# Kernel tuning notes

Measured on AMD Instinct MI355X. Metric: run time of the kernel, lower is better.

The kernel has to match this reference:

```python
import jax, jax.numpy as jnp
import numpy as np
import math

B = 8192       # batch (tokens)
HID = 4096     # hidden size
H = 32         # num query heads
KV = 8         # num kv heads
GQA = H // KV  # 4
D = 128        # head dim
RBIT = 128     # hash bits
QKV = (H + 2 * KV) * D  # 6144


def setup_inputs() -> dict:
    key = jax.random.key(0)
    k1, k2, k3 = jax.random.split(key, 3)
    hidden = jax.random.normal(k1, (B, HID), jnp.float32)
    proj_w = jax.random.normal(k2, (HID, QKV), jnp.float32) * 0.02
    proj_b = jnp.zeros((QKV,), jnp.float32)
    # xavier_uniform init for hash weight [D, RBIT]
    limit = math.sqrt(6.0 / (D + RBIT))
    hash_w = jax.random.uniform(k3, (D, RBIT), jnp.float32, -limit, limit)
    return {"hidden": hidden, "proj_w": proj_w, "proj_b": proj_b, "hash_w": hash_w}


def reference(hidden, proj_w, proj_b, hash_w):
    # fused qkv projection
    qkv = hidden @ proj_w + proj_b                     # [B, QKV]
    q = qkv[:, : H * D].reshape(B, H, D)               # [B, H, D]
    k = qkv[:, H * D : (H + KV) * D].reshape(B, KV, 1, D)
    k = jnp.broadcast_to(k, (B, KV, GQA, D)).reshape(B, H, D)  # GQA expand

    inv_sqrt_d = 1.0 / math.sqrt(D)
    attn_weights = jnp.einsum("bhd,bhd->bh", q, k) * inv_sqrt_d  # with_norm=True

    # hash codes: BinaryStochastic (training mode): (tanh(x)+1)/2
    q_code = (jnp.tanh(q @ hash_w) + 1.0) * 0.5        # [B, H, RBIT]
    k_code = (jnp.tanh(k @ hash_w) + 1.0) * 0.5
    ham_dist = jnp.abs(q_code - k_code).sum(axis=-1)   # [B, H]
    ham_weights = 1.0 - 2.0 * ham_dist / RBIT

    # with_norm: scale by |q| |k| / sqrt(D)
    q_norm = jnp.linalg.norm(q, axis=-1)
    k_norm = jnp.linalg.norm(k, axis=-1)
    ham_weights = ham_weights * q_norm * k_norm * inv_sqrt_d

    return attn_weights.reshape(-1), ham_weights.reshape(-1)
```

## Files before the change

### kernel.cpp

```cpp
#include <hip/hip_runtime.h>
#include <hip/hip_bf16.h>
#include <cstdint>
#include <cstddef>

#define B_TOK 8192
#define HID   4096
#define NH    32
#define NKV   8
#define DH    128
#define RB    128
#define KDIM  4096
#define NOUT  5120
#define QKVW  6144

typedef __bf16 bf16x8 __attribute__((ext_vector_type(8)));
typedef __bf16 bf16x4 __attribute__((ext_vector_type(4)));
typedef float  f32x4  __attribute__((ext_vector_type(4)));

__device__ __forceinline__ void async_ld16(const void* g, void* l) {
  __builtin_amdgcn_global_load_lds(
      (__attribute__((address_space(1))) void*)(g),
      (__attribute__((address_space(3))) void*)(l), 16, 0, 0);
}

__device__ __forceinline__ float code_of(float x) {
  const float e = exp2f(x * -2.885390081777927f);
  return __builtin_amdgcn_rcpf(1.0f + e);
}


#define NB_HID  16384
#define NB_WT   5120
#define NB_HASH 64

__global__ void prep_kernel(const float* __restrict__ hidden, __bf16* __restrict__ Abf,
                            const float* __restrict__ W, __bf16* __restrict__ Wt,
                            const float* __restrict__ hw, __bf16* __restrict__ hwT) {
  __shared__ float t[64][65];
  const int bx  = blockIdx.x;
  const int tid = threadIdx.x;

  if (bx < NB_HID) {
    const int i = bx * 256 + tid;
    const float4 v0 = ((const float4*)hidden)[2 * i];
    const float4 v1 = ((const float4*)hidden)[2 * i + 1];
    bf16x8 o;
    o[0] = (__bf16)v0.x; o[1] = (__bf16)v0.y; o[2] = (__bf16)v0.z; o[3] = (__bf16)v0.w;
    o[4] = (__bf16)v1.x; o[5] = (__bf16)v1.y; o[6] = (__bf16)v1.z; o[7] = (__bf16)v1.w;
    ((bf16x8*)Abf)[i] = o;
  } else if (bx < NB_HID + NB_WT) {
    const int bt = bx - NB_HID;
    const int n0 = (bt % 80) * 64;
    const int k0 = (bt / 80) * 64;
    const int c  = tid & 63;
    const int r0 = tid >> 6;
#pragma unroll
    for (int j = 0; j < 16; ++j) {
      const int r = r0 + j * 4;
      t[r][c] = W[(size_t)(k0 + r) * QKVW + n0 + c];
    }
    __syncthreads();
#pragma unroll
    for (int j = 0; j < 16; ++j) {
      const int n = r0 + j * 4;
      Wt[(size_t)(n0 + n) * KDIM + k0 + c] = (__bf16)t[c][n];
    }
  } else {
    const int idx = (bx - NB_HID - NB_WT) * 256 + tid;
    const int r = idx >> 7;
    const int d = idx & 127;
    hwT[r * RB + d] = (__bf16)hw[(size_t)d * RB + r];
  }
}


__global__ void gemm_qk(const __bf16* __restrict__ A,
                        const __bf16* __restrict__ Bt,
                        const float* __restrict__ bias,
                        __bf16* __restrict__ C) {
  __shared__ __bf16 As[128 * 32];
  __shared__ __bf16 Bs[128 * 32];

  const int tid  = threadIdx.x;
  const int lane = tid & 63;
  const int wave = tid >> 6;
  const int m0 = blockIdx.y * 128;
  const int n0 = blockIdx.x * 128;
  const int waveM = (wave >> 1) * 64;
  const int waveN = (wave & 1) * 64;

  const int srow  = lane >> 2;
  const int selem = (lane & 3) * 8;

  const __bf16* ga0 = A + (size_t)(m0 + wave * 16 + srow) * KDIM + selem;
  const __bf16* ga1 = ga0 + (size_t)64 * KDIM;
  const __bf16* gb0 = Bt + (size_t)(n0 + wave * 16 + srow) * KDIM + selem;
  const __bf16* gb1 = gb0 + (size_t)64 * KDIM;
  __bf16* la0 = As + wave * 512;
  __bf16* la1 = As + (wave + 4) * 512;
  __bf16* lb0 = Bs + wave * 512;
  __bf16* lb1 = Bs + (wave + 4) * 512;

  const int fr = lane & 15;
  const int fk = (lane >> 4) * 8;

  f32x4 acc[4][4] = {};

  for (int kt = 0; kt < KDIM / 32; ++kt) {
    const int k0 = kt * 32;
    async_ld16(ga0 + k0, la0);
    async_ld16(ga1 + k0, la1);
    async_ld16(gb0 + k0, lb0);
    async_ld16(gb1 + k0, lb1);
    __syncthreads();

    bf16x8 af[4], bfr[4];
#pragma unroll
    for (int mi = 0; mi < 4; ++mi)
      af[mi] = *(const bf16x8*)(As + (waveM + mi * 16 + fr) * 32 + fk);
#pragma unroll
    for (int ni = 0; ni < 4; ++ni)
      bfr[ni] = *(const bf16x8*)(Bs + (waveN + ni * 16 + fr) * 32 + fk);
#pragma unroll
    for (int mi = 0; mi < 4; ++mi)
#pragma unroll
      for (int ni = 0; ni < 4; ++ni)
        acc[mi][ni] = __builtin_amdgcn_mfma_f32_16x16x32_bf16(af[mi], bfr[ni],
                                                              acc[mi][ni], 0, 0, 0);
    __syncthreads();
  }

  const int cl = lane & 15;
  const int rq = (lane >> 4) * 4;
#pragma unroll
  for (int ni = 0; ni < 4; ++ni) {
    const int gn = n0 + waveN + ni * 16 + cl;
    const float bb = bias[gn];
#pragma unroll
    for (int mi = 0; mi < 4; ++mi) {
      const int gm = m0 + waveM + mi * 16 + rq;
#pragma unroll
      for (int r = 0; r < 4; ++r)
        C[(size_t)(gm + r) * NOUT + gn] = (__bf16)(acc[mi][ni][r] + bb);
    }
  }
}


__global__ void phase2_kernel(const __bf16* __restrict__ QK,
                              const __bf16* __restrict__ hwT,
                              float* __restrict__ out) {
  __shared__ __bf16 As[48][136];
  __shared__ float code[40][132];
  __shared__ float rednorm[40];
  __shared__ float reddot[32];

  const int tid  = threadIdx.x;
  const int lane = tid & 63;
  const int wave = tid >> 6;
  const int b = blockIdx.x;

  const __bf16* src = QK + (size_t)b * NOUT;
  for (int i = tid; i < 640; i += 256) {
    const int row = i >> 4;
    const int col = (i & 15) * 8;
    *(uint4*)(&As[row][col]) = *(const uint4*)(src + i * 8);
  }

  const int fr = lane & 15;
  const int fk = (lane >> 4) * 8;
  bf16x8 bf[2][4];
#pragma unroll
  for (int nn = 0; nn < 2; ++nn) {
    const int ni = wave + nn * 4;
#pragma unroll
    for (int ks = 0; ks < 4; ++ks)
      bf[nn][ks] = *(const bf16x8*)(hwT + (size_t)(ni * 16 + fr) * RB + ks * 32 + fk);
  }
  __syncthreads();

#pragma unroll
  for (int mi = 0; mi < 3; ++mi) {
    bf16x8 af[4];
#pragma unroll
    for (int ks = 0; ks < 4; ++ks)
      af[ks] = *(const bf16x8*)(&As[mi * 16 + fr][ks * 32 + fk]);
#pragma unroll
    for (int nn = 0; nn < 2; ++nn) {
      const int ni = wave + nn * 4;
      f32x4 acc = {0.f, 0.f, 0.f, 0.f};
#pragma unroll
      for (int ks = 0; ks < 4; ++ks)
        acc = __builtin_amdgcn_mfma_f32_16x16x32_bf16(af[ks], bf[nn][ks], acc, 0, 0, 0);
      const int row0 = mi * 16 + (lane >> 4) * 4;
      const int col  = ni * 16 + (lane & 15);
#pragma unroll
      for (int r = 0; r < 4; ++r) {
        const int row = row0 + r;
        if (row < 40) code[row][col] = code_of(acc[r]);
      }
    }
  }

  {
    const int q = lane >> 4;
    const int c = lane & 15;
    const int ti = (wave == 1 || wave == 3) ? 1 : 0;
    const int tj = (wave >= 2) ? 2 : ti;
    bf16x8 fa[4], fb[4];
#pragma unroll
    for (int ks = 0; ks < 4; ++ks) {
      fa[ks] = *(const bf16x8*)(&As[ti * 16 + fr][ks * 32 + fk]);
      fb[ks] = *(const bf16x8*)(&As[tj * 16 + fr][ks * 32 + fk]);
    }
    f32x4 g = {0.f, 0.f, 0.f, 0.f};
#pragma unroll
    for (int ks = 0; ks < 4; ++ks)
      g = __builtin_amdgcn_mfma_f32_16x16x32_bf16(fa[ks], fb[ks], g, 0, 0, 0);
    if (ti == tj) {
      if ((c >> 2) == q) rednorm[ti * 16 + c] = g[c & 3];
    } else {
      if (c == ti * 4 + q) {
#pragma unroll
        for (int r = 0; r < 4; ++r) reddot[ti * 16 + q * 4 + r] = g[r];
      }
    }
    if (wave == 0) {
      bf16x8 fc[4];
#pragma unroll
      for (int ks = 0; ks < 4; ++ks)
        fc[ks] = *(const bf16x8*)(&As[32 + fr][ks * 32 + fk]);
      f32x4 g2 = {0.f, 0.f, 0.f, 0.f};
#pragma unroll
      for (int ks = 0; ks < 4; ++ks)
        g2 = __builtin_amdgcn_mfma_f32_16x16x32_bf16(fc[ks], fc[ks], g2, 0, 0, 0);
      if ((c >> 2) == q && c < 8) rednorm[32 + c] = g2[c & 3];
    }
  }
  __syncthreads();

  const int h   = tid >> 3;
  const int sub = tid & 7;
  const int kr  = 32 + (h >> 2);
  float s = 0.f;
#pragma unroll
  for (int j = 0; j < 16; ++j) {
    const int c = sub + 8 * j;
    s += fabsf(code[h][c] - code[kr][c]);
  }
  s += __shfl_down(s, 4, 8);
  s += __shfl_down(s, 2, 8);
  s += __shfl_down(s, 1, 8);
  if (sub == 0) {
    const float invsq = 0.08838834764831843f;
    out[(size_t)b * NH + h] = reddot[h] * invsq;
    const float hamw = (1.0f - s * (1.0f / 64.0f)) *
                       sqrtf(rednorm[h]) * sqrtf(rednorm[kr]) * invsq;
    out[(size_t)(B_TOK * NH) + (size_t)b * NH + h] = hamw;
  }
}


extern "C" void kernel_launch(void* const* d_in, const int* in_sizes, int n_in,
                              void* d_out, int out_size, void* d_ws, size_t ws_size,
                              hipStream_t stream) {
  const float* hidden = (const float*)d_in[0];
  const float* proj_w = (const float*)d_in[1];
  const float* proj_b = (const float*)d_in[2];
  const float* hash_w = (const float*)d_in[3];
  float* out = (float*)d_out;

  char* w = (char*)d_ws;
  __bf16* Abf = (__bf16*)(w);
  __bf16* Wt  = (__bf16*)(w + 67108864);
  __bf16* QK  = (__bf16*)(w + 67108864 + 41943040);
  __bf16* hwT = (__bf16*)(w + 67108864 + 41943040 + 83886080);

  prep_kernel<<<NB_HID + NB_WT + NB_HASH, 256, 0, stream>>>(hidden, Abf, proj_w, Wt,
                                                            hash_w, hwT);
  gemm_qk<<<dim3(NOUT / 128, B_TOK / 128), 256, 0, stream>>>(Abf, Wt, proj_b, QK);
  phase2_kernel<<<B_TOK, 256, 0, stream>>>(QK, hwT, out);
}
```

Before: 685.0 us.

## Vectorize weight transpose, double K-step per barrier, remap GEMM tiles per XCD

The weight transpose in the prep kernel now reads float4 rows and writes bf16x8 vectors instead of scalar elements, to cut the number of memory transactions. The GEMM main loop now loads a K=64 slab per iteration into two LDS buffers, halving the number of barrier pairs per tile. The block index is also remapped so that each XCD handles a contiguous group of N tiles, aiming to improve L2 reuse of the weight tiles. The price is twice the LDS per block, which may lower occupancy, and a tile mapping that assumes a 40-wide grid.

New measurement: 630.7 us. 7.9% less time.

```diff
diff --git a/kernel.cpp b/kernel.cpp
--- a/kernel.cpp
+++ b/kernel.cpp
@@ -52,18 +52,25 @@
     const int bt = bx - NB_HID;
     const int n0 = (bt % 80) * 64;
     const int k0 = (bt / 80) * 64;
-    const int c  = tid & 63;
-    const int r0 = tid >> 6;
-#pragma unroll
-    for (int j = 0; j < 16; ++j) {
-      const int r = r0 + j * 4;
-      t[r][c] = W[(size_t)(k0 + r) * QKVW + n0 + c];
+    const int c4 = tid & 15;
+    const int rr = tid >> 4;
+#pragma unroll
+    for (int j = 0; j < 4; ++j) {
+      const int r = rr + j * 16;
+      const float4 v = *(const float4*)&W[(size_t)(k0 + r) * QKVW + n0 + c4 * 4];
+      t[r][c4 * 4 + 0] = v.x; t[r][c4 * 4 + 1] = v.y;
+      t[r][c4 * 4 + 2] = v.z; t[r][c4 * 4 + 3] = v.w;
     }
     __syncthreads();
-#pragma unroll
-    for (int j = 0; j < 16; ++j) {
-      const int n = r0 + j * 4;
-      Wt[(size_t)(n0 + n) * KDIM + k0 + c] = (__bf16)t[c][n];
+    const int c8 = tid & 7;
+    const int nn = tid >> 3;
+#pragma unroll
+    for (int jj = 0; jj < 2; ++jj) {
+      const int n = nn + jj * 32;
+      bf16x8 o;
+#pragma unroll
+      for (int i = 0; i < 8; ++i) o[i] = (__bf16)t[c8 * 8 + i][n];
+      *(bf16x8*)&Wt[(size_t)(n0 + n) * KDIM + k0 + c8 * 8] = o;
     }
   } else {
     const int idx = (bx - NB_HID - NB_WT) * 256 + tid;
@@ -78,14 +85,19 @@
                         const __bf16* __restrict__ Bt,
                         const float* __restrict__ bias,
                         __bf16* __restrict__ C) {
-  __shared__ __bf16 As[128 * 32];
-  __shared__ __bf16 Bs[128 * 32];
+  __shared__ __bf16 As[2][128 * 32];
+  __shared__ __bf16 Bs[2][128 * 32];
 
   const int tid  = threadIdx.x;
   const int lane = tid & 63;
   const int wave = tid >> 6;
-  const int m0 = blockIdx.y * 128;
-  const int n0 = blockIdx.x * 128;
+
+  const int lin = blockIdx.y * 40 + blockIdx.x;
+  const int xcd = lin & 7;
+  const int seq = lin >> 3;
+  const int n0 = (xcd * 5 + (seq % 5)) * 128;
+  const int m0 = (seq / 5) * 128;
+
   const int waveM = (wave >> 1) * 64;
   const int waveN = (wave & 1) * 64;
 
@@ -96,37 +108,44 @@
   const __bf16* ga1 = ga0 + (size_t)64 * KDIM;
   const __bf16* gb0 = Bt + (size_t)(n0 + wave * 16 + srow) * KDIM + selem;
   const __bf16* gb1 = gb0 + (size_t)64 * KDIM;
-  __bf16* la0 = As + wave * 512;
-  __bf16* la1 = As + (wave + 4) * 512;
-  __bf16* lb0 = Bs + wave * 512;
-  __bf16* lb1 = Bs + (wave + 4) * 512;
+  __bf16* la0 = &As[0][wave * 512];
+  __bf16* la1 = &As[0][(wave + 4) * 512];
+  __bf16* lb0 = &Bs[0][wave * 512];
+  __bf16* lb1 = &Bs[0][(wave + 4) * 512];
+  __bf16* la0b = &As[1][wave * 512];
+  __bf16* la1b = &As[1][(wave + 4) * 512];
+  __bf16* lb0b = &Bs[1][wave * 512];
+  __bf16* lb1b = &Bs[1][(wave + 4) * 512];
 
   const int fr = lane & 15;
   const int fk = (lane >> 4) * 8;
 
   f32x4 acc[4][4] = {};
 
-  for (int kt = 0; kt < KDIM / 32; ++kt) {
-    const int k0 = kt * 32;
-    async_ld16(ga0 + k0, la0);
-    async_ld16(ga1 + k0, la1);
-    async_ld16(gb0 + k0, lb0);
-    async_ld16(gb1 + k0, lb1);
+  for (int kt = 0; kt < KDIM / 64; ++kt) {
+    const int k0 = kt * 64;
+    async_ld16(ga0 + k0, la0);  async_ld16(ga0 + k0 + 32, la0b);
+    async_ld16(ga1 + k0, la1);  async_ld16(ga1 + k0 + 32, la1b);
+    async_ld16(gb0 + k0, lb0);  async_ld16(gb0 + k0 + 32, lb0b);
+    async_ld16(gb1 + k0, lb1);  async_ld16(gb1 + k0 + 32, lb1b);
     __syncthreads();
 
-    bf16x8 af[4], bfr[4];
-#pragma unroll
-    for (int mi = 0; mi < 4; ++mi)
-      af[mi] = *(const bf16x8*)(As + (waveM + mi * 16 + fr) * 32 + fk);
-#pragma unroll
-    for (int ni = 0; ni < 4; ++ni)
-      bfr[ni] = *(const bf16x8*)(Bs + (waveN + ni * 16 + fr) * 32 + fk);
-#pragma unroll
-    for (int mi = 0; mi < 4; ++mi)
+#pragma unroll
+    for (int ks = 0; ks < 2; ++ks) {
+      bf16x8 af[4], bfr[4];
+#pragma unroll
+      for (int mi = 0; mi < 4; ++mi)
+        af[mi] = *(const bf16x8*)(&As[ks][(waveM + mi * 16 + fr) * 32 + fk]);
 #pragma unroll
       for (int ni = 0; ni < 4; ++ni)
-        acc[mi][ni] = __builtin_amdgcn_mfma_f32_16x16x32_bf16(af[mi], bfr[ni],
-                                                              acc[mi][ni], 0, 0, 0);
+        bfr[ni] = *(const bf16x8*)(&Bs[ks][(waveN + ni * 16 + fr) * 32 + fk]);
+#pragma unroll
+      for (int mi = 0; mi < 4; ++mi)
+#pragma unroll
+        for (int ni = 0; ni < 4; ++ni)
+          acc[mi][ni] = __builtin_amdgcn_mfma_f32_16x16x32_bf16(af[mi], bfr[ni],
+                                                                acc[mi][ni], 0, 0, 0);
+    }
     __syncthreads();
   }
 
```
